# Kernel optimization log

Measured on AMD Instinct MI355X. Metric: run time of the kernel, lower is better.

Reference implementation:

```python
import jax, jax.numpy as jnp
import numpy as np

B, P, F, H, NF, E, V, L = 128, 196, 2048, 512, 512, 512, 10000, 20
T = L - 1
EPS = 1e-5  # BatchNorm eps (eval mode, running_mean=0, running_var=1)


def setup_inputs() -> dict:
    key = jax.random.key(0)
    ks = jax.random.split(key, 16)

    def kaiming(k, out_d, in_d):
        return jax.random.normal(k, (out_d, in_d), jnp.float32) * np.float32(np.sqrt(2.0 / in_d))

    encoder_feat = jax.random.normal(ks[0], (B, P, F), jnp.float32)
    gt_captions = jax.random.randint(ks[1], (B, L), 0, V)
    # lengths in [2, L], sorted descending (torch code assumes this), max forced to L
    captions_len = jnp.sort(jax.random.randint(ks[2], (B,), 2, L + 1))[::-1].at[0].set(L)

    emb = jax.random.uniform(ks[3], (V, E), jnp.float32, -0.1, 0.1)
    Wfa = kaiming(ks[4], NF, F); bfa = jnp.zeros((NF,), jnp.float32)
    Wha = kaiming(ks[5], NF, H); bha = jnp.zeros((NF,), jnp.float32)
    Wv = kaiming(ks[6], 1, NF); bv = jnp.zeros((1,), jnp.float32)
    Wh0 = kaiming(ks[7], H, F); bh0 = jnp.zeros((H,), jnp.float32)
    Wc0 = kaiming(ks[8], H, F); bc0 = jnp.zeros((H,), jnp.float32)
    gamma_h = jnp.ones((H,), jnp.float32); beta_h = jnp.zeros((H,), jnp.float32)
    gamma_c = jnp.ones((H,), jnp.float32); beta_c = jnp.zeros((H,), jnp.float32)
    Wfb = kaiming(ks[9], F, H); bfb = jnp.zeros((F,), jnp.float32)
    s = np.float32(1.0 / np.sqrt(H))  # torch LSTMCell default init range
    Wih = jax.random.uniform(ks[10], (4 * H, E + F), jnp.float32, -s, s)
    Whh = jax.random.uniform(ks[11], (4 * H, H), jnp.float32, -s, s)
    bih = jax.random.uniform(ks[12], (4 * H,), jnp.float32, -s, s)
    bhh = jax.random.uniform(ks[13], (4 * H,), jnp.float32, -s, s)
    Wfc = kaiming(ks[14], V, H); bfc = jnp.zeros((V,), jnp.float32)

    return dict(encoder_feat=encoder_feat, emb=emb, Wfa=Wfa, bfa=bfa, Wha=Wha, bha=bha,
                Wv=Wv, bv=bv, Wh0=Wh0, bh0=bh0, Wc0=Wc0, bc0=bc0,
                gamma_h=gamma_h, beta_h=beta_h, gamma_c=gamma_c, beta_c=beta_c,
                Wfb=Wfb, bfb=bfb, Wih=Wih, Whh=Whh, bih=bih, bhh=bhh,
                Wfc=Wfc, bfc=bfc, gt_captions=gt_captions, captions_len=captions_len)


def reference(encoder_feat, emb, Wfa, bfa, Wha, bha, Wv, bv, Wh0, bh0, Wc0, bc0,
              gamma_h, beta_h, gamma_c, beta_c, Wfb, bfb, Wih, Whh, bih, bhh,
              Wfc, bfc, gt_captions, captions_len):
    # Eval-mode semantics: dropout = identity, weight-drop inactive,
    # BatchNorm1d uses default running stats (mean=0, var=1).
    def bn(x, g, b):
        return g * (x / jnp.sqrt(1.0 + EPS)) + b

    feat = encoder_feat.mean(axis=1)                       # [B, F]
    h = bn(jax.nn.sigmoid(feat @ Wh0.T + bh0), gamma_h, beta_h)
    c = bn(jax.nn.sigmoid(feat @ Wc0.T + bc0), gamma_c, beta_c)

    # attention key projection is h-independent: hoist out of the time loop
    feat_att = jnp.einsum('bpf,nf->bpn', encoder_feat, Wfa) + bfa  # [B, P, NF]
    emb_seq = emb[gt_captions]                                      # [B, L, E]

    # ragged batch handled by masking (equivalent to torch's [:batch_size_t] slicing)
    mask = (jnp.arange(T)[:, None] < (captions_len - 1)[None, :]).astype(encoder_feat.dtype)  # [T, B]
    xs = (jnp.swapaxes(emb_seq[:, :T], 0, 1), mask)

    def step(carry, xt):
        h, c = carry
        emb_t, m = xt                                      # [B, E], [B]
        att = jax.nn.relu(feat_att + (h @ Wha.T + bha)[:, None, :])
        e = jnp.einsum('bpn,n->bp', att, Wv[0]) + bv[0]    # [B, P]
        alpha = jax.nn.softmax(e, axis=1)
        context = jnp.einsum('bpf,bp->bf', encoder_feat, alpha)
        gate = jax.nn.sigmoid(h @ Wfb.T + bfb)             # [B, F]
        x = jnp.concatenate([emb_t, gate * context], axis=1)
        gates = x @ Wih.T + bih + h @ Whh.T + bhh          # [B, 4H]
        i, f, g, o = jnp.split(gates, 4, axis=1)
        c_new = jax.nn.sigmoid(f) * c + jax.nn.sigmoid(i) * jnp.tanh(g)
        h_new = jax.nn.sigmoid(o) * jnp.tanh(c_new)
        preds = h_new @ Wfc.T + bfc                        # [B, V]
        mf = m[:, None]
        return (h_new, c_new), (preds * mf, alpha * mf)

    _, (preds, alphas) = jax.lax.scan(step, (h, c), xs)
    predictions = jnp.swapaxes(preds, 0, 1)                # [B, T, V]
    alphas = jnp.swapaxes(alphas, 0, 1)                    # [B, T, P]
    return predictions, alphas
```

## Files before the change

kernel.cpp:

```cpp
#include <hip/hip_runtime.h>
#include <cstdint>
#include <cstddef>

#define B_  128
#define P_  196
#define F_  2048
#define H_  512
#define NF_ 512
#define E_  512
#define V_  10000
#define L_  20
#define T_  19
#define NPAD_ 10112
#define NCP_ (2560 + NPAD_)

typedef short s8v __attribute__((ext_vector_type(8)));
typedef float f32x4 __attribute__((ext_vector_type(4)));
typedef unsigned short u16x8 __attribute__((ext_vector_type(8)));

__device__ __forceinline__ float sigf(float x) { return 1.0f / (1.0f + expf(-x)); }
__device__ __forceinline__ ushort f2b(float f) {
    unsigned u = __builtin_bit_cast(unsigned, f);
    u += 0x7fff + ((u >> 16) & 1);
    return (ushort)(u >> 16);
}
__device__ __forceinline__ float b2f(ushort h) {
    unsigned u = ((unsigned)h) << 16;
    return __builtin_bit_cast(float, u);
}

__global__ __launch_bounds__(256)
void cast_mat(const float* __restrict__ s, ushort* __restrict__ d,
              long long total, int cols, int sld, int srows) {
    long long i4 = ((long long)blockIdx.x * 256 + threadIdx.x) * 4;
    if (i4 >= total) return;
    int n = (int)(i4 / cols);
    int k = (int)(i4 - (long long)n * cols);
    float4 v = make_float4(0.f, 0.f, 0.f, 0.f);
    if (n < srows) v = *(const float4*)(s + (size_t)n * sld + k);
    ushort4 o;
    o.x = f2b(v.x); o.y = f2b(v.y); o.z = f2b(v.z); o.w = f2b(v.w);
    *(ushort4*)(d + i4) = o;
}

__global__ __launch_bounds__(256)
void cast_perm(const float* __restrict__ s, ushort* __restrict__ d,
               int cols, int sld) {
    int idx = blockIdx.x * 256 + threadIdx.x;
    int i4 = idx * 4;
    int n = i4 / cols;
    int k = i4 - n * cols;
    int r = (n & 3) * H_ + (n >> 2);
    float4 v = *(const float4*)(s + (size_t)r * sld + k);
    ushort4 o;
    o.x = f2b(v.x); o.y = f2b(v.y); o.z = f2b(v.z); o.w = f2b(v.w);
    *(ushort4*)(d + (size_t)n * cols + k) = o;
}

__global__ __launch_bounds__(256)
void build_bg(const float* __restrict__ bih, const float* __restrict__ bhh,
              float* __restrict__ bg) {
    int n = blockIdx.x * 256 + threadIdx.x;
    int r = (n & 3) * H_ + (n >> 2);
    bg[n] = bih[r] + bhh[r];
}

__global__ __launch_bounds__(256)
void build_bcp(const float* __restrict__ bha, const float* __restrict__ bfb,
               const float* __restrict__ bfc, float* __restrict__ bcp) {
    int n = blockIdx.x * 256 + threadIdx.x;
    if (n >= NCP_) return;
    float v;
    if (n < 512) v = bha[n];
    else if (n < 2560) v = bfb[n - 512];
    else { int r = n - 2560; v = (r < V_) ? bfc[r] : 0.0f; }
    bcp[n] = v;
}

__global__ __launch_bounds__(256)
void mean_cast_kernel(const float* __restrict__ enc, ushort* __restrict__ encb,
                      float* __restrict__ feat) {
    int b = blockIdx.x >> 3;
    int f = ((blockIdx.x & 7) << 8) + threadIdx.x;
    const float* p = enc + (size_t)b * P_ * F_ + f;
    ushort* pb = encb + (size_t)b * P_ * F_ + f;
    float s = 0.0f;
    for (int q = 0; q < P_; q++) {
        float v = p[(size_t)q * F_];
        pb[(size_t)q * F_] = f2b(v);
        s += v;
    }
    feat[b * F_ + f] = s * (1.0f / 196.0f);
}

__global__ __launch_bounds__(256) void mean_kernel(const float* __restrict__ enc,
                                                   float* __restrict__ feat) {
    int b = blockIdx.x >> 3;
    int f = ((blockIdx.x & 7) << 8) + threadIdx.x;
    const float* p = enc + (size_t)b * P_ * F_ + f;
    float s = 0.0f;
    for (int q = 0; q < P_; q++) s += p[(size_t)q * F_];
    feat[b * F_ + f] = s * (1.0f / 196.0f);
}

__global__ __launch_bounds__(256) void gather_b(const float* __restrict__ emb,
                                                const int* __restrict__ gt,
                                                ushort* __restrict__ embx) {
    int idx = blockIdx.x * 256 + threadIdx.x;
    int i4 = idx * 4;
    int e = i4 & (E_ - 1);
    int bt = i4 >> 9;
    int b = bt / T_, t = bt - b * T_;
    int tok = gt[b * L_ + t];
    float4 v = *(const float4*)(emb + (size_t)tok * E_ + e);
    ushort4 o;
    o.x = f2b(v.x); o.y = f2b(v.y); o.z = f2b(v.z); o.w = f2b(v.w);
    *(ushort4*)(embx + i4) = o;
}

__global__ __launch_bounds__(256)
void gemm_biasb(const float* __restrict__ A, int lda,
                const float* __restrict__ W, int ldw,
                const float* __restrict__ bias,
                ushort* __restrict__ C, long long ldc,
                int M, int N, int K) {
    __shared__ float As[16][65];
    __shared__ float Ws[16][65];
    const int tid = threadIdx.x;
    const int m0 = blockIdx.y << 6;
    const int n0 = blockIdx.x << 6;
    const int row = tid >> 2;
    const int kq  = (tid & 3) << 2;
    const int ty = tid >> 4, tx = tid & 15;
    float acc[4][4] = {};
    for (int k0 = 0; k0 < K; k0 += 16) {
        float4 av = make_float4(0.f, 0.f, 0.f, 0.f);
        float4 wv = make_float4(0.f, 0.f, 0.f, 0.f);
        int m = m0 + row;
        if (m < M) av = *(const float4*)(A + (size_t)m * lda + k0 + kq);
        int n = n0 + row;
        if (n < N) wv = *(const float4*)(W + (size_t)n * ldw + k0 + kq);
        __syncthreads();
        As[kq + 0][row] = av.x; As[kq + 1][row] = av.y;
        As[kq + 2][row] = av.z; As[kq + 3][row] = av.w;
        Ws[kq + 0][row] = wv.x; Ws[kq + 1][row] = wv.y;
        Ws[kq + 2][row] = wv.z; Ws[kq + 3][row] = wv.w;
        __syncthreads();
#pragma unroll
        for (int k = 0; k < 16; k++) {
            float a[4], w[4];
#pragma unroll
            for (int i = 0; i < 4; i++) a[i] = As[k][(ty << 2) + i];
#pragma unroll
            for (int j = 0; j < 4; j++) w[j] = Ws[k][(tx << 2) + j];
#pragma unroll
            for (int i = 0; i < 4; i++)
#pragma unroll
                for (int j = 0; j < 4; j++)
                    acc[i][j] = fmaf(a[i], w[j], acc[i][j]);
        }
    }
#pragma unroll
    for (int i = 0; i < 4; i++) {
        int m = m0 + (ty << 2) + i;
        if (m >= M) continue;
#pragma unroll
        for (int j = 0; j < 4; j++) {
            int n = n0 + (tx << 2) + j;
            if (n >= N) continue;
            C[(size_t)m * ldc + n] = f2b(acc[i][j] + bias[n]);
        }
    }
}

enum { MEPI_NONE = 0, MEPI_BIAS = 1, MEPI_BIASB = 2, MEPI_COMBOPRED = 3 };

__device__ __forceinline__ void stage_tile(const ushort* __restrict__ g, int ld,
                                           int row0, int k0, ushort* lds,
                                           int rows, int w, int l) {
    int nchunk = rows >> 4;
    for (int c = w; c < nchunk; c += 4) {
        int flat = c * 1024 + l * 16;
        int r = flat >> 6;
        int ce = (flat & 63) >> 1;
        const ushort* gp = g + (size_t)(row0 + r) * ld + (k0 + ce);
        __builtin_amdgcn_global_load_lds(
            (const __attribute__((address_space(1))) void*)gp,
            (__attribute__((address_space(3))) void*)(lds + c * 512),
            16, 0, 0);
    }
}

template <int BM, int EPI, int DUAL>
__global__ __launch_bounds__(256)
void mfma_gemm(const ushort* __restrict__ A1, int lda1,
               const ushort* __restrict__ W1, int ldw1, int K1,
               const ushort* __restrict__ A2, int lda2,
               const ushort* __restrict__ W2, int ldw2, int K2,
               const float* __restrict__ bias, void* __restrict__ Cout, long long ldc,
               void* __restrict__ Cout2,
               int M, int N,
               const int* __restrict__ clen, int tcur) {
    __shared__ ushort As[BM * 32];
    __shared__ ushort Bs[128 * 32];
    const int tid = threadIdx.x;
    const int w = tid >> 6, l = tid & 63;
    const int wr = w >> 1, wc = w & 1;
    constexpr int WM = BM / 2;
    constexpr int AF = WM / 16;
    const int m0 = blockIdx.y * BM;
    const int n0 = blockIdx.x * 128;
    const int lrow = l & 15, lk8 = (l >> 4) * 8;
    const int kz = blockIdx.z, nzz = gridDim.z;

    f32x4 acc[AF][4] = {};

    for (int pass = 0; pass < 1 + DUAL; pass++) {
        const ushort* A = pass ? A2 : A1;
        const ushort* W = pass ? W2 : W1;
        const int lda = pass ? lda2 : lda1;
        const int ldw = pass ? ldw2 : ldw1;
        const int K  = pass ? K2 : K1;
        const int chunk = K / nzz;
        const int kbeg = kz * chunk;
        const int kend = kbeg + chunk;
        for (int k0 = kbeg; k0 < kend; k0 += 32) {
            __syncthreads();
            stage_tile(A, lda, m0, k0, As, BM, w, l);
            stage_tile(W, ldw, n0, k0, Bs, 128, w, l);
            __syncthreads();
            s8v af[AF], bf[4];
#pragma unroll
            for (int i = 0; i < AF; i++)
                af[i] = *(const s8v*)(As + (wr * WM + i * 16 + lrow) * 32 + lk8);
#pragma unroll
            for (int j = 0; j < 4; j++)
                bf[j] = *(const s8v*)(Bs + (wc * 64 + j * 16 + lrow) * 32 + lk8);
#pragma unroll
            for (int i = 0; i < AF; i++)
#pragma unroll
                for (int j = 0; j < 4; j++)
                    acc[i][j] = __builtin_amdgcn_mfma_f32_16x16x32_bf16(
                        af[i], bf[j], acc[i][j], 0, 0, 0);
        }
    }

    float* Cz = (float*)Cout + (size_t)kz * (size_t)M * ldc;
#pragma unroll
    for (int i = 0; i < AF; i++) {
        int rb = m0 + wr * WM + i * 16 + (l >> 4) * 4;
#pragma unroll
        for (int j = 0; j < 4; j++) {
            int n = n0 + wc * 64 + j * 16 + (l & 15);
            if (n >= N) continue;
#pragma unroll
            for (int r = 0; r < 4; r++) {
                int m = rb + r;
                float v = acc[i][j][r];
                if (EPI == MEPI_NONE) {
                    Cz[(size_t)m * ldc + n] = v;
                } else if (EPI == MEPI_BIAS) {
                    ((float*)Cout)[(size_t)m * ldc + n] = v + bias[n];
                } else if (EPI == MEPI_BIASB) {
                    ((ushort*)Cout)[(size_t)m * ldc + n] = f2b(v + bias[n]);
                } else if (EPI == MEPI_COMBOPRED) {
                    if (n < 2560) {
                        ((float*)Cout)[(size_t)m * 2560 + n] = v + bias[n];
                    } else {
                        int col = n - 2560;
                        if (col < V_) {
                            float mk = (tcur < clen[m] - 1) ? 1.0f : 0.0f;
                            ((float*)Cout2)[(size_t)m * ((long long)T_ * V_) + col] =
                                (v + bias[n]) * mk;
                        }
                    }
                }
            }
        }
    }
}

__global__ __launch_bounds__(256)
void h0c0_final(const float* __restrict__ part,
                const float* __restrict__ b0,
                const float* __restrict__ g0,
                const float* __restrict__ bt0,
                float* __restrict__ cbuf, ushort* __restrict__ hb) {
    int idx = blockIdx.x * 256 + threadIdx.x;
    int b = idx >> 9, j = idx & 511;
    const float rbn = 1.0f / sqrtf(1.0f + 1e-5f);
    float sh = b0[j], sc = b0[j + 512];
    for (int z = 0; z < 4; z++) {
        sh += part[((size_t)z * B_ + b) * 1024 + j];
        sc += part[((size_t)z * B_ + b) * 1024 + j + 512];
    }
    float hv = g0[j] * (sigf(sh) * rbn) + bt0[j];
    float cv = g0[j + 512] * (sigf(sc) * rbn) + bt0[j + 512];
    cbuf[idx] = cv;
    hb[idx] = f2b(hv);
}

template <int BF>
__global__ __launch_bounds__(256)
void attn_ctx(const void* __restrict__ encv, const ushort* __restrict__ fa,
              const float* __restrict__ combo, const float* __restrict__ Wv,
              float* __restrict__ alphas_out, const int* __restrict__ clen,
              ushort* __restrict__ gctxb, int t) {
    int b = blockIdx.x >> 1;
    int half = blockIdx.x & 1;
    int tid = threadIdx.x;
    int w = tid >> 6, l = tid & 63;
    __shared__ float eS[256];
    __shared__ float red[256];
    __shared__ float pc[128 * 8];
    const float* hap = combo + (size_t)b * 2560;
    float ha8[8], wv8[8];
#pragma unroll
    for (int i = 0; i < 8; i++) { ha8[i] = hap[l * 8 + i]; wv8[i] = Wv[l * 8 + i]; }
    eS[tid] = -1e30f;
    __syncthreads();
    const ushort* fab = fa + (size_t)b * P_ * NF_;
    for (int p = w; p < P_; p += 4) {
        const ushort* fp = fab + (size_t)p * NF_ + l * 8;
        ushort4 u0 = *(const ushort4*)fp;
        ushort4 u1 = *(const ushort4*)(fp + 4);
        float s = 0.0f, v;
        v = b2f(u0.x) + ha8[0]; v = v > 0.f ? v : 0.f; s = fmaf(v, wv8[0], s);
        v = b2f(u0.y) + ha8[1]; v = v > 0.f ? v : 0.f; s = fmaf(v, wv8[1], s);
        v = b2f(u0.z) + ha8[2]; v = v > 0.f ? v : 0.f; s = fmaf(v, wv8[2], s);
        v = b2f(u0.w) + ha8[3]; v = v > 0.f ? v : 0.f; s = fmaf(v, wv8[3], s);
        v = b2f(u1.x) + ha8[4]; v = v > 0.f ? v : 0.f; s = fmaf(v, wv8[4], s);
        v = b2f(u1.y) + ha8[5]; v = v > 0.f ? v : 0.f; s = fmaf(v, wv8[5], s);
        v = b2f(u1.z) + ha8[6]; v = v > 0.f ? v : 0.f; s = fmaf(v, wv8[6], s);
        v = b2f(u1.w) + ha8[7]; v = v > 0.f ? v : 0.f; s = fmaf(v, wv8[7], s);
#pragma unroll
        for (int off = 32; off > 0; off >>= 1) s += __shfl_down(s, off, 64);
        if (l == 0) eS[p] = s;
    }
    __syncthreads();
    float ev = eS[tid];
    red[tid] = ev;
    __syncthreads();
    for (int s = 128; s > 0; s >>= 1) {
        if (tid < s) red[tid] = fmaxf(red[tid], red[tid + s]);
        __syncthreads();
    }
    float mx = red[0];
    __syncthreads();
    float ex = expf(ev - mx);
    red[tid] = ex;
    __syncthreads();
    for (int s = 128; s > 0; s >>= 1) {
        if (tid < s) red[tid] += red[tid + s];
        __syncthreads();
    }
    float inv = 1.0f / red[0];
    float a = ex * inv;
    __syncthreads();
    eS[tid] = a;
    if (half == 0 && tid < P_) {
        float m = (t < clen[b] - 1) ? 1.0f : 0.0f;
        alphas_out[((size_t)b * T_ + t) * P_ + tid] = a * m;
    }
    __syncthreads();

    int tl = tid & 127;
    int pr = tid >> 7;
    int pp0 = pr * 98;
    int f0 = (half << 10) + tl * 8;
    float s[8] = {};
    if (BF) {
        const ushort* ep = (const ushort*)encv + (size_t)b * P_ * F_ +
                           (size_t)pp0 * F_ + f0;
        for (int p = 0; p < 98; p++) {
            u16x8 u = *(const u16x8*)(ep + (size_t)p * F_);
            float al = eS[pp0 + p];
#pragma unroll
            for (int i = 0; i < 8; i++) s[i] = fmaf(al, b2f(u[i]), s[i]);
        }
    } else {
        const float* ep = (const float*)encv + (size_t)b * P_ * F_ +
                          (size_t)pp0 * F_ + f0;
        for (int p = 0; p < 98; p++) {
            float4 u0 = *(const float4*)(ep + (size_t)p * F_);
            float4 u1 = *(const float4*)(ep + (size_t)p * F_ + 4);
            float al = eS[pp0 + p];
            s[0] = fmaf(al, u0.x, s[0]); s[1] = fmaf(al, u0.y, s[1]);
            s[2] = fmaf(al, u0.z, s[2]); s[3] = fmaf(al, u0.w, s[3]);
            s[4] = fmaf(al, u1.x, s[4]); s[5] = fmaf(al, u1.y, s[5]);
            s[6] = fmaf(al, u1.z, s[6]); s[7] = fmaf(al, u1.w, s[7]);
        }
    }
    if (pr) {
#pragma unroll
        for (int i = 0; i < 8; i++) pc[tl * 8 + i] = s[i];
    }
    __syncthreads();
    if (!pr) {
        const float* gp = combo + (size_t)b * 2560 + 512 + f0;
        float4 ga = *(const float4*)gp;
        float4 gb = *(const float4*)(gp + 4);
        float gv[8] = {ga.x, ga.y, ga.z, ga.w, gb.x, gb.y, gb.z, gb.w};
        ushort o[8];
#pragma unroll
        for (int i = 0; i < 8; i++)
            o[i] = f2b(sigf(gv[i]) * (s[i] + pc[tl * 8 + i]));
        *(u16x8*)(gctxb + (size_t)b * F_ + f0) = *(u16x8*)o;
    }
}

__global__ __launch_bounds__(256)
void lstm_perm(const float* __restrict__ gatesP,
               const float* __restrict__ embprojP,
               const float* __restrict__ bg,
               float* __restrict__ cbuf, ushort* __restrict__ hout, int t) {
    int idx = blockIdx.x * 256 + threadIdx.x;
    int b = idx >> 9, j = idx & (H_ - 1);
    int n0 = j * 4;
    float4 g = *(const float4*)(embprojP + ((size_t)b * T_ + t) * 2048 + n0);
    float4 bgv = *(const float4*)(bg + n0);
    g.x += bgv.x; g.y += bgv.y; g.z += bgv.z; g.w += bgv.w;
#pragma unroll
    for (int z = 0; z < 4; z++) {
        float4 p = *(const float4*)(gatesP + ((size_t)z * B_ + b) * 2048 + n0);
        g.x += p.x; g.y += p.y; g.z += p.z; g.w += p.w;
    }
    float cn = sigf(g.y) * cbuf[idx] + sigf(g.x) * tanhf(g.z);
    float hn = sigf(g.w) * tanhf(cn);
    cbuf[idx] = cn;
    hout[idx] = f2b(hn);
}

extern "C" void kernel_launch(void* const* d_in, const int* in_sizes, int n_in,
                              void* d_out, int out_size, void* d_ws, size_t ws_size,
                              hipStream_t stream) {
    const float* enc = (const float*)d_in[0];
    const float* emb = (const float*)d_in[1];
    const float* Wfa = (const float*)d_in[2];
    const float* bfa = (const float*)d_in[3];
    const float* Wha = (const float*)d_in[4];
    const float* bha = (const float*)d_in[5];
    const float* Wv  = (const float*)d_in[6];
    const float* Wh0 = (const float*)d_in[8];
    const float* bh0 = (const float*)d_in[9];
    const float* Wc0 = (const float*)d_in[10];
    const float* bc0 = (const float*)d_in[11];
    const float* gh  = (const float*)d_in[12];
    const float* bth = (const float*)d_in[13];
    const float* gc  = (const float*)d_in[14];
    const float* btc = (const float*)d_in[15];
    const float* Wfb = (const float*)d_in[16];
    const float* bfb = (const float*)d_in[17];
    const float* Wih = (const float*)d_in[18];
    const float* Whh = (const float*)d_in[19];
    const float* bih = (const float*)d_in[20];
    const float* bhh = (const float*)d_in[21];
    const float* Wfc = (const float*)d_in[22];
    const float* bfc = (const float*)d_in[23];
    const int* gt   = (const int*)d_in[24];
    const int* clen = (const int*)d_in[25];

    float* out_pred  = (float*)d_out;
    float* out_alpha = out_pred + (size_t)B_ * T_ * V_;

    char* wp = (char*)d_ws;
    auto alloc = [&](size_t bytes) {
        char* p = wp;
        wp += (bytes + 255) & ~(size_t)255;
        return p;
    };
    float*  feat     = (float*)alloc((size_t)B_ * F_ * 4);
    float*  cbuf     = (float*)alloc((size_t)B_ * H_ * 4);
    float*  combo    = (float*)alloc((size_t)B_ * 2560 * 4);
    float*  embprojP = (float*)alloc((size_t)B_ * T_ * 2048 * 4);
    float*  gatesP   = (float*)alloc((size_t)4 * B_ * 2048 * 4);
    float*  hcpart   = (float*)alloc((size_t)4 * B_ * 1024 * 4);
    float*  bcp      = (float*)alloc((size_t)NCP_ * 4);
    float*  bg       = (float*)alloc(2048 * 4);
    float*  b0comb   = (float*)alloc(1024 * 4);
    float*  g0comb   = (float*)alloc(1024 * 4);
    float*  bt0comb  = (float*)alloc(1024 * 4);
    ushort* hb0      = (ushort*)alloc((size_t)B_ * H_ * 2);
    ushort* hb1      = (ushort*)alloc((size_t)B_ * H_ * 2);
    ushort* gctxb    = (ushort*)alloc((size_t)B_ * F_ * 2);
    ushort* embxb    = (ushort*)alloc((size_t)B_ * T_ * E_ * 2);
    ushort* fattb    = (ushort*)alloc((size_t)B_ * P_ * NF_ * 2);
    ushort* featb    = (ushort*)alloc((size_t)B_ * F_ * 2);
    ushort* Wfab     = (ushort*)alloc((size_t)NF_ * F_ * 2);
    ushort* WihEbP   = (ushort*)alloc((size_t)2048 * E_ * 2);
    ushort* WihFbP   = (ushort*)alloc((size_t)2048 * F_ * 2);
    ushort* WhhbP    = (ushort*)alloc((size_t)2048 * H_ * 2);
    ushort* Wcp      = (ushort*)alloc((size_t)NCP_ * H_ * 2);
    ushort* W0comb   = (ushort*)alloc((size_t)1024 * F_ * 2);
    ushort* encb     = (ushort*)alloc((size_t)B_ * P_ * F_ * 2);
    const bool big = ((size_t)(wp - (char*)d_ws) <= ws_size);

    auto castM = [&](const float* s, ushort* d, long long rows, int cols, int sld, int srows) {
        long long total = rows * (long long)cols;
        cast_mat<<<(int)((total + 1023) / 1024), 256, 0, stream>>>(s, d, total, cols, sld, srows);
    };

    castM(Wfa, Wfab, NF_, F_, F_, NF_);
    cast_perm<<<(2048 * E_) / 1024, 256, 0, stream>>>(Wih, WihEbP, E_, E_ + F_);
    cast_perm<<<(2048 * F_) / 1024, 256, 0, stream>>>(Wih + E_, WihFbP, F_, E_ + F_);
    cast_perm<<<(2048 * H_) / 1024, 256, 0, stream>>>(Whh, WhhbP, H_, H_);
    castM(Wha, Wcp, NF_, H_, H_, NF_);
    castM(Wfb, Wcp + (size_t)512 * H_, F_, H_, H_, F_);
    castM(Wfc, Wcp + (size_t)2560 * H_, NPAD_, H_, H_, V_);
    castM(Wh0, W0comb, H_, F_, F_, H_);
    castM(Wc0, W0comb + (size_t)H_ * F_, H_, F_, F_, H_);
    build_bg<<<2048 / 256, 256, 0, stream>>>(bih, bhh, bg);
    build_bcp<<<(NCP_ + 255) / 256, 256, 0, stream>>>(bha, bfb, bfc, bcp);
    hipMemcpyAsync(b0comb, bh0, H_ * 4, hipMemcpyDeviceToDevice, stream);
    hipMemcpyAsync(b0comb + H_, bc0, H_ * 4, hipMemcpyDeviceToDevice, stream);
    hipMemcpyAsync(g0comb, gh, H_ * 4, hipMemcpyDeviceToDevice, stream);
    hipMemcpyAsync(g0comb + H_, gc, H_ * 4, hipMemcpyDeviceToDevice, stream);
    hipMemcpyAsync(bt0comb, bth, H_ * 4, hipMemcpyDeviceToDevice, stream);
    hipMemcpyAsync(bt0comb + H_, btc, H_ * 4, hipMemcpyDeviceToDevice, stream);

    if (big) mean_cast_kernel<<<B_ * 8, 256, 0, stream>>>(enc, encb, feat);
    else     mean_kernel<<<B_ * 8, 256, 0, stream>>>(enc, feat);
    castM(feat, featb, B_, F_, F_, B_);
    mfma_gemm<32, MEPI_NONE, 0><<<dim3(1024 / 128, B_ / 32, 4), 256, 0, stream>>>(
        featb, F_, W0comb, F_, F_, nullptr, 0, nullptr, 0, 0,
        nullptr, hcpart, 1024, nullptr, B_, 1024, nullptr, 0);
    h0c0_final<<<(B_ * H_) / 256, 256, 0, stream>>>(hcpart, b0comb, g0comb, bt0comb, cbuf, hb0);
    gather_b<<<(B_ * T_ * E_) / 1024, 256, 0, stream>>>(emb, gt, embxb);

    if (big) {
        mfma_gemm<128, MEPI_BIASB, 0><<<dim3(NF_ / 128, (B_ * P_) / 128, 1), 256, 0, stream>>>(
            encb, F_, Wfab, F_, F_, nullptr, 0, nullptr, 0, 0,
            bfa, fattb, NF_, nullptr, B_ * P_, NF_, nullptr, 0);
    } else {
        gemm_biasb<<<dim3(NF_ / 64, (B_ * P_) / 64), 256, 0, stream>>>(
            enc, F_, Wfa, F_, bfa, fattb, NF_, B_ * P_, NF_, F_);
    }
    mfma_gemm<128, MEPI_NONE, 0><<<dim3(2048 / 128, (B_ * T_) / 128, 1), 256, 0, stream>>>(
        embxb, E_, WihEbP, E_, E_, nullptr, 0, nullptr, 0, 0,
        nullptr, embprojP, 2048, nullptr, B_ * T_, 2048, nullptr, 0);

    mfma_gemm<32, MEPI_BIAS, 0><<<dim3(2560 / 128, B_ / 32, 1), 256, 0, stream>>>(
        hb0, H_, Wcp, H_, H_, nullptr, 0, nullptr, 0, 0,
        bcp, combo, 2560, nullptr, B_, 2560, nullptr, 0);

    for (int t = 0; t < T_; t++) {
        ushort* hin  = (t & 1) ? hb1 : hb0;
        ushort* hout = (t & 1) ? hb0 : hb1;
        if (big) attn_ctx<1><<<B_ * 2, 256, 0, stream>>>(encb, fattb, combo, Wv,
                                                         out_alpha, clen, gctxb, t);
        else     attn_ctx<0><<<B_ * 2, 256, 0, stream>>>(enc, fattb, combo, Wv,
                                                         out_alpha, clen, gctxb, t);
        mfma_gemm<32, MEPI_NONE, 1><<<dim3(2048 / 128, B_ / 32, 4), 256, 0, stream>>>(
            gctxb, F_, WihFbP, F_, F_, hin, H_, WhhbP, H_, H_,
            nullptr, gatesP, 2048, nullptr, B_, 2048, nullptr, 0);
        lstm_perm<<<(B_ * H_) / 256, 256, 0, stream>>>(
            gatesP, embprojP, bg, cbuf, hout, t);
        mfma_gemm<32, MEPI_COMBOPRED, 0><<<dim3(NCP_ / 128, B_ / 32, 1), 256, 0, stream>>>(
            hout, H_, Wcp, H_, H_, nullptr, 0, nullptr, 0, 0,
            bcp, combo, 2560, out_pred + (size_t)t * V_, B_, NCP_, clen, t);
    }
}
```

Before: 2.072 ms.

## Hoist vocab projection out of recurrence into one batched GEMM; add XCD block swizzle

Every hidden state is now kept in one history buffer instead of ping-pong buffers. The per-step combined GEMM is cut to only the attention/gate columns (2560), and the vocabulary projection runs once after the loop as a single large GEMM over all B*T rows with a 128-row tile, writing masked predictions directly. The aim is to stop re-streaming the 10000x512 Wfc weight on every one of the 19 serial steps with a tiny M=128 GEMM, and to shorten the critical path of each step. A block-index swizzle spreading workgroups across the 8 XCDs is also added for the large GEMMs. The cost is extra workspace for the hidden-state history.

```diff
diff --git a/kernel.cpp b/kernel.cpp
--- a/kernel.cpp
+++ b/kernel.cpp
@@ -12,7 +12,6 @@
 #define L_  20
 #define T_  19
 #define NPAD_ 10112
-#define NCP_ (2560 + NPAD_)
 
 typedef short s8v __attribute__((ext_vector_type(8)));
 typedef float f32x4 __attribute__((ext_vector_type(4)));
@@ -65,6 +64,7 @@
     bg[n] = bih[r] + bhh[r];
 }
 
+#define NCP_ (2560 + NPAD_)
 __global__ __launch_bounds__(256)
 void build_bcp(const float* __restrict__ bha, const float* __restrict__ bfb,
                const float* __restrict__ bfc, float* __restrict__ bcp) {
@@ -173,7 +173,7 @@
     }
 }
 
-enum { MEPI_NONE = 0, MEPI_BIAS = 1, MEPI_BIASB = 2, MEPI_COMBOPRED = 3 };
+enum { MEPI_NONE = 0, MEPI_BIAS = 1, MEPI_BIASB = 2, MEPI_PREDS = 3 };
 
 __device__ __forceinline__ void stage_tile(const ushort* __restrict__ g, int ld,
                                            int row0, int k0, ushort* lds,
@@ -191,7 +191,7 @@
     }
 }
 
-template <int BM, int EPI, int DUAL>
+template <int BM, int EPI, int DUAL, int SWZ = 0>
 __global__ __launch_bounds__(256)
 void mfma_gemm(const ushort* __restrict__ A1, int lda1,
                const ushort* __restrict__ W1, int ldw1, int K1,
@@ -208,8 +208,19 @@
     const int wr = w >> 1, wc = w & 1;
     constexpr int WM = BM / 2;
     constexpr int AF = WM / 16;
-    const int m0 = blockIdx.y * BM;
-    const int n0 = blockIdx.x * 128;
+    int bx = blockIdx.x, by = blockIdx.y;
+    if (SWZ) {
+        const int gx = gridDim.x;
+        const int nwg = gx * gridDim.y;
+        const int fid = by * gx + bx;
+        const int q = nwg >> 3, r = nwg & 7;
+        const int xcd = fid & 7, idx = fid >> 3;
+        const int nf = (xcd < r ? xcd * (q + 1)
+                                : r * (q + 1) + (xcd - r) * q) + idx;
+        bx = nf % gx; by = nf / gx;
+    }
+    const int m0 = by * BM;
+    const int n0 = bx * 128;
     const int lrow = l & 15, lk8 = (l >> 4) * 8;
     const int kz = blockIdx.z, nzz = gridDim.z;
 
@@ -263,16 +274,13 @@
                     ((float*)Cout)[(size_t)m * ldc + n] = v + bias[n];
                 } else if (EPI == MEPI_BIASB) {
                     ((ushort*)Cout)[(size_t)m * ldc + n] = f2b(v + bias[n]);
-                } else if (EPI == MEPI_COMBOPRED) {
-                    if (n < 2560) {
-                        ((float*)Cout)[(size_t)m * 2560 + n] = v + bias[n];
-                    } else {
-                        int col = n - 2560;
-                        if (col < V_) {
-                            float mk = (tcur < clen[m] - 1) ? 1.0f : 0.0f;
-                            ((float*)Cout2)[(size_t)m * ((long long)T_ * V_) + col] =
-                                (v + bias[n]) * mk;
-                        }
+                } else if (EPI == MEPI_PREDS) {
+                    if (n < V_) {
+                        int bb = m & (B_ - 1);
+                        int tt = m >> 7;
+                        float mk = (tt < clen[bb] - 1) ? 1.0f : 0.0f;
+                        ((float*)Cout)[((size_t)bb * T_ + tt) * (size_t)V_ + n] =
+                            (v + bias[n]) * mk;
                     }
                 }
             }
@@ -480,8 +488,7 @@
     float*  b0comb   = (float*)alloc(1024 * 4);
     float*  g0comb   = (float*)alloc(1024 * 4);
     float*  bt0comb  = (float*)alloc(1024 * 4);
-    ushort* hb0      = (ushort*)alloc((size_t)B_ * H_ * 2);
-    ushort* hb1      = (ushort*)alloc((size_t)B_ * H_ * 2);
+    ushort* hall     = (ushort*)alloc((size_t)(T_ + 1) * B_ * H_ * 2);
     ushort* gctxb    = (ushort*)alloc((size_t)B_ * F_ * 2);
     ushort* embxb    = (ushort*)alloc((size_t)B_ * T_ * E_ * 2);
     ushort* fattb    = (ushort*)alloc((size_t)B_ * P_ * NF_ * 2);
@@ -524,11 +531,11 @@
     mfma_gemm<32, MEPI_NONE, 0><<<dim3(1024 / 128, B_ / 32, 4), 256, 0, stream>>>(
         featb, F_, W0comb, F_, F_, nullptr, 0, nullptr, 0, 0,
         nullptr, hcpart, 1024, nullptr, B_, 1024, nullptr, 0);
-    h0c0_final<<<(B_ * H_) / 256, 256, 0, stream>>>(hcpart, b0comb, g0comb, bt0comb, cbuf, hb0);
+    h0c0_final<<<(B_ * H_) / 256, 256, 0, stream>>>(hcpart, b0comb, g0comb, bt0comb, cbuf, hall);
     gather_b<<<(B_ * T_ * E_) / 1024, 256, 0, stream>>>(emb, gt, embxb);
 
     if (big) {
-        mfma_gemm<128, MEPI_BIASB, 0><<<dim3(NF_ / 128, (B_ * P_) / 128, 1), 256, 0, stream>>>(
+        mfma_gemm<128, MEPI_BIASB, 0, 1><<<dim3(NF_ / 128, (B_ * P_) / 128, 1), 256, 0, stream>>>(
             encb, F_, Wfab, F_, F_, nullptr, 0, nullptr, 0, 0,
             bfa, fattb, NF_, nullptr, B_ * P_, NF_, nullptr, 0);
     } else {
@@ -540,12 +547,12 @@
         nullptr, embprojP, 2048, nullptr, B_ * T_, 2048, nullptr, 0);
 
     mfma_gemm<32, MEPI_BIAS, 0><<<dim3(2560 / 128, B_ / 32, 1), 256, 0, stream>>>(
-        hb0, H_, Wcp, H_, H_, nullptr, 0, nullptr, 0, 0,
+        hall, H_, Wcp, H_, H_, nullptr, 0, nullptr, 0, 0,
         bcp, combo, 2560, nullptr, B_, 2560, nullptr, 0);
 
     for (int t = 0; t < T_; t++) {
-        ushort* hin  = (t & 1) ? hb1 : hb0;
-        ushort* hout = (t & 1) ? hb0 : hb1;
+        ushort* hin  = hall + (size_t)t * B_ * H_;
+        ushort* hout = hall + (size_t)(t + 1) * B_ * H_;
         if (big) attn_ctx<1><<<B_ * 2, 256, 0, stream>>>(encb, fattb, combo, Wv,
                                                          out_alpha, clen, gctxb, t);
         else     attn_ctx<0><<<B_ * 2, 256, 0, stream>>>(enc, fattb, combo, Wv,
@@ -555,8 +562,13 @@
             nullptr, gatesP, 2048, nullptr, B_, 2048, nullptr, 0);
         lstm_perm<<<(B_ * H_) / 256, 256, 0, stream>>>(
             gatesP, embprojP, bg, cbuf, hout, t);
-        mfma_gemm<32, MEPI_COMBOPRED, 0><<<dim3(NCP_ / 128, B_ / 32, 1), 256, 0, stream>>>(
+        mfma_gemm<32, MEPI_BIAS, 0><<<dim3(2560 / 128, B_ / 32, 1), 256, 0, stream>>>(
             hout, H_, Wcp, H_, H_, nullptr, 0, nullptr, 0, 0,
-            bcp, combo, 2560, out_pred + (size_t)t * V_, B_, NCP_, clen, t);
-    }
-}
+            bcp, combo, 2560, nullptr, B_, 2560, nullptr, 0);
+    }
+
+    mfma_gemm<128, MEPI_PREDS, 0, 1><<<dim3(NPAD_ / 128, (B_ * T_) / 128, 1), 256, 0, stream>>>(
+        hall + (size_t)B_ * H_, H_, Wcp + (size_t)2560 * H_, H_, H_,
+        nullptr, 0, nullptr, 0, 0,
+        bcp + 2560, out_pred, V_, nullptr, B_ * T_, NPAD_, clen, 0);
+}
```

After: 1.989 ms. 4.0% less time.
